# Kernel optimization log

Hardware: AMD Instinct MI355X
Metric: run time of the kernel (lower is better)

Reference implementation:

```python
import jax, jax.numpy as jnp
import numpy as np

B, CLEN, QLEN, H = 16, 4096, 512, 256


def setup_inputs() -> dict:
    key = jax.random.key(0)
    ks = jax.random.split(key, 8)
    scale = 1.0 / np.sqrt(H)
    return {
        "c": jax.random.normal(ks[0], (B, CLEN, H), dtype=jnp.float32),
        "q": jax.random.normal(ks[1], (B, QLEN, H), dtype=jnp.float32),
        "w_c": jax.random.normal(ks[2], (H,), dtype=jnp.float32) * scale,
        "b_c": jax.random.normal(ks[3], (), dtype=jnp.float32) * scale,
        "w_q": jax.random.normal(ks[4], (H,), dtype=jnp.float32) * scale,
        "b_q": jax.random.normal(ks[5], (), dtype=jnp.float32) * scale,
        "w_cq": jax.random.normal(ks[6], (H,), dtype=jnp.float32) * scale,
        "b_cq": jax.random.normal(ks[7], (), dtype=jnp.float32) * scale,
    }


def reference(c, q, w_c, b_c, w_q, b_q, w_cq, b_cq):
    # Trilinear similarity: s[b,i,j] = c_i.w_c + q_j.w_q + sum_d w_cq[d]*c[b,i,d]*q[b,j,d] + biases
    cq = jnp.einsum("bid,bjd->bij", c * w_cq, q) + b_cq          # (B, c_len, q_len)
    s = (c @ w_c + b_c)[:, :, None] + (q @ w_q + b_q)[:, None, :] + cq
    # context-to-query attention
    a = jax.nn.softmax(s, axis=2)                                  # (B, c_len, q_len)
    c2q_att = jnp.einsum("bij,bjd->bid", a, q)                     # (B, c_len, H)
    # query-to-context attention (max over queries, softmax over context)
    b_att = jax.nn.softmax(jnp.max(s, axis=2), axis=1)             # (B, c_len)
    q2c_att = jnp.einsum("bi,bid->bd", b_att, c)[:, None, :]       # (B, 1, H)
    q2c_att = jnp.broadcast_to(q2c_att, c.shape)                   # (B, c_len, H)
    x = jnp.concatenate([c, c2q_att, c * c2q_att, c * q2c_att], axis=2)
    return x  # (B, c_len, 4*H)
```

## Files before the change

kernel.cpp:

```cpp
#include <hip/hip_runtime.h>
#include <hip/hip_fp16.h>

constexpr int NB = 16;
constexpr int CL = 4096;
constexpr int QL = 512;
constexpr int HD = 256;

typedef _Float16 f16x8 __attribute__((ext_vector_type(8)));
typedef _Float16 f16x4 __attribute__((ext_vector_type(4)));
typedef float    f32x4 __attribute__((ext_vector_type(4)));


__global__ void k_prep_q(const float* __restrict__ q, const float* __restrict__ w_q,
                         const float* __restrict__ b_q, const float* __restrict__ w_cq,
                         const float* __restrict__ b_cq,
                         _Float16* __restrict__ qph, float* __restrict__ qd2) {
    int row  = blockIdx.x * 4 + (threadIdx.x >> 6);
    int lane = threadIdx.x & 63;
    float4 qv  = ((const float4*)(q + (size_t)row * HD))[lane];
    float4 wq  = ((const float4*)w_q)[lane];
    float4 wcq = ((const float4*)w_cq)[lane];
    f16x4 hv = {(_Float16)(qv.x * wcq.x), (_Float16)(qv.y * wcq.y),
                (_Float16)(qv.z * wcq.z), (_Float16)(qv.w * wcq.w)};
    *(f16x4*)(qph + (size_t)row * HD + lane * 4) = hv;
    float s = qv.x * wq.x + qv.y * wq.y + qv.z * wq.z + qv.w * wq.w;
    #pragma unroll
    for (int off = 32; off; off >>= 1) s += __shfl_down(s, off, 64);
    if (lane == 0) qd2[row] = s + b_q[0] + b_cq[0];
}

__global__ void k_cdot(const float* __restrict__ c, const float* __restrict__ w_c,
                       const float* __restrict__ b_c, float* __restrict__ cdot) {
    int row  = blockIdx.x * 4 + (threadIdx.x >> 6);
    int lane = threadIdx.x & 63;
    float4 cv = ((const float4*)(c + (size_t)row * HD))[lane];
    float4 wv = ((const float4*)w_c)[lane];
    float s = cv.x * wv.x + cv.y * wv.y + cv.z * wv.z + cv.w * wv.w;
    #pragma unroll
    for (int off = 32; off; off >>= 1) s += __shfl_down(s, off, 64);
    if (lane == 0) cdot[row] = s + b_c[0];
}

__global__ void k_tq(const float* __restrict__ q, _Float16* __restrict__ qth) {
    __shared__ float tile[64][65];
    int b  = blockIdx.z;
    int d0 = blockIdx.x * 64;
    int j0 = blockIdx.y * 64;
    int t  = threadIdx.x;
    int rr = t >> 4, cseg = t & 15;
    #pragma unroll
    for (int p = 0; p < 4; ++p) {
        int r = rr + p * 16;
        float4 v = *(const float4*)(q + ((size_t)b * QL + j0 + r) * HD + d0 + cseg * 4);
        tile[r][cseg * 4 + 0] = v.x; tile[r][cseg * 4 + 1] = v.y;
        tile[r][cseg * 4 + 2] = v.z; tile[r][cseg * 4 + 3] = v.w;
    }
    __syncthreads();
    #pragma unroll
    for (int p = 0; p < 4; ++p) {
        int dr = rr + p * 16;
        f16x4 hv = {(_Float16)tile[cseg * 4 + 0][dr], (_Float16)tile[cseg * 4 + 1][dr],
                    (_Float16)tile[cseg * 4 + 2][dr], (_Float16)tile[cseg * 4 + 3][dr]};
        *(f16x4*)(qth + ((size_t)b * HD + d0 + dr) * QL + j0 + cseg * 4) = hv;
    }
}

__launch_bounds__(512, 4)
__global__ void k_fused(const float* __restrict__ c, const _Float16* __restrict__ qph,
                        const float* __restrict__ qd2, const _Float16* __restrict__ qth,
                        float* __restrict__ rowmax, float* __restrict__ x) {
    __shared__ __align__(1024) char smem[65536];

    const int b  = blockIdx.y;
    const int i0 = blockIdx.x * 64;
    const int t  = threadIdx.x;
    const int wave = t >> 6;
    const int ln   = t & 15;
    const int quad = (t >> 4) & 3;
    const int jw   = wave;

    f32x4 acc[4][4];
    #pragma unroll
    for (int mt = 0; mt < 4; ++mt)
        #pragma unroll
        for (int nt = 0; nt < 4; ++nt) acc[mt][nt] = (f32x4){0.f, 0.f, 0.f, 0.f};

    for (int dc = 0; dc < 4; ++dc) {
        __syncthreads();
        {
            const int row = t >> 3, seg = t & 7;
            #pragma unroll
            for (int p = 0; p < 8; ++p) {
                int j = row + p * 64;
                f16x8 hv = *(const f16x8*)(qph + ((size_t)b * QL + j) * HD + dc * 64 + seg * 8);
                int byte = (j << 7) + (seg << 4);
                byte ^= (j & 7) << 4;
                *(f16x8*)(smem + byte) = hv;
            }
        }
        __syncthreads();
        #pragma unroll
        for (int ks = 0; ks < 2; ++ks) {
            f16x8 bf[4];
            #pragma unroll
            for (int nt = 0; nt < 4; ++nt) {
                const float* src = c + ((size_t)b * CL + i0 + nt * 16 + ln) * HD
                                     + dc * 64 + ks * 32 + quad * 8;
                float4 v0 = *(const float4*)src;
                float4 v1 = *(const float4*)(src + 4);
                bf[nt] = (f16x8){(_Float16)v0.x, (_Float16)v0.y, (_Float16)v0.z, (_Float16)v0.w,
                                 (_Float16)v1.x, (_Float16)v1.y, (_Float16)v1.z, (_Float16)v1.w};
            }
            #pragma unroll
            for (int mt = 0; mt < 4; ++mt) {
                int j = jw * 64 + mt * 16 + ln;
                int byte = (j << 7) + (ks * 64 + quad * 16);
                byte ^= (j & 7) << 4;
                f16x8 af = *(const f16x8*)(smem + byte);
                #pragma unroll
                for (int nt = 0; nt < 4; ++nt)
                    acc[mt][nt] = __builtin_amdgcn_mfma_f32_16x16x32_f16(af, bf[nt], acc[mt][nt], 0, 0, 0);
            }
        }
    }

    float m[4];
    #pragma unroll
    for (int nt = 0; nt < 4; ++nt) m[nt] = -1e30f;
    #pragma unroll
    for (int mt = 0; mt < 4; ++mt) {
        float4 qv = *(const float4*)(qd2 + b * QL + jw * 64 + mt * 16 + quad * 4);
        #pragma unroll
        for (int nt = 0; nt < 4; ++nt) {
            acc[mt][nt][0] += qv.x; acc[mt][nt][1] += qv.y;
            acc[mt][nt][2] += qv.z; acc[mt][nt][3] += qv.w;
            m[nt] = fmaxf(m[nt], fmaxf(fmaxf(acc[mt][nt][0], acc[mt][nt][1]),
                                       fmaxf(acc[mt][nt][2], acc[mt][nt][3])));
        }
    }
    #pragma unroll
    for (int nt = 0; nt < 4; ++nt) {
        m[nt] = fmaxf(m[nt], __shfl_xor(m[nt], 16, 64));
        m[nt] = fmaxf(m[nt], __shfl_xor(m[nt], 32, 64));
    }
    __syncthreads();
    float* redM = (float*)smem;
    float* redZ = (float*)(smem + 2048);
    if (quad == 0) {
        #pragma unroll
        for (int nt = 0; nt < 4; ++nt) redM[jw * 64 + nt * 16 + ln] = m[nt];
    }
    __syncthreads();
    #pragma unroll
    for (int nt = 0; nt < 4; ++nt) {
        int ri = nt * 16 + ln;
        float mm = redM[ri];
        #pragma unroll
        for (int w = 1; w < 8; ++w) mm = fmaxf(mm, redM[w * 64 + ri]);
        m[nt] = mm;
    }
    if (jw == 0 && quad == 0) {
        #pragma unroll
        for (int nt = 0; nt < 4; ++nt)
            rowmax[(size_t)b * CL + i0 + nt * 16 + ln] = m[nt];
    }
    float z[4] = {0.f, 0.f, 0.f, 0.f};
    #pragma unroll
    for (int mt = 0; mt < 4; ++mt)
        #pragma unroll
        for (int nt = 0; nt < 4; ++nt) {
            #pragma unroll
            for (int r = 0; r < 4; ++r) {
                float e = __expf(acc[mt][nt][r] - m[nt]);
                acc[mt][nt][r] = e;
                z[nt] += e;
            }
        }
    #pragma unroll
    for (int nt = 0; nt < 4; ++nt) {
        z[nt] += __shfl_xor(z[nt], 16, 64);
        z[nt] += __shfl_xor(z[nt], 32, 64);
    }
    if (quad == 0) {
        #pragma unroll
        for (int nt = 0; nt < 4; ++nt) redZ[jw * 64 + nt * 16 + ln] = z[nt];
    }
    __syncthreads();
    float inv[4];
    #pragma unroll
    for (int nt = 0; nt < 4; ++nt) {
        int ri = nt * 16 + ln;
        float zz = redZ[ri];
        #pragma unroll
        for (int w = 1; w < 8; ++w) zz += redZ[w * 64 + ri];
        inv[nt] = 1.0f / zz;
    }
    __syncthreads();

    #pragma unroll
    for (int mt = 0; mt < 4; ++mt) {
        int jcol = jw * 64 + mt * 16 + quad * 4;
        #pragma unroll
        for (int nt = 0; nt < 4; ++nt) {
            int i = nt * 16 + ln;
            f16x4 hv = {(_Float16)(acc[mt][nt][0] * inv[nt]),
                        (_Float16)(acc[mt][nt][1] * inv[nt]),
                        (_Float16)(acc[mt][nt][2] * inv[nt]),
                        (_Float16)(acc[mt][nt][3] * inv[nt])};
            int byte = (i << 10) + (jcol << 1);
            byte ^= (i & 7) << 4;
            *(f16x4*)(smem + byte) = hv;
        }
    }
    __syncthreads();

    const int iw = wave >> 2;
    const int dw = wave & 3;
    f32x4 acc2[2][4];
    #pragma unroll
    for (int it = 0; it < 2; ++it)
        #pragma unroll
        for (int dt = 0; dt < 4; ++dt) acc2[it][dt] = (f32x4){0.f, 0.f, 0.f, 0.f};

    const _Float16* qthb = qth + (size_t)b * HD * QL;
    #pragma unroll 4
    for (int kc = 0; kc < 16; ++kc) {
        f16x8 af[2], bf[4];
        #pragma unroll
        for (int it = 0; it < 2; ++it) {
            int i = iw * 32 + it * 16 + ln;
            int byte = (i << 10) + (kc * 64 + quad * 16);
            byte ^= (i & 7) << 4;
            af[it] = *(const f16x8*)(smem + byte);
        }
        #pragma unroll
        for (int dt = 0; dt < 4; ++dt)
            bf[dt] = *(const f16x8*)(qthb + (size_t)(dw * 64 + dt * 16 + ln) * QL
                                     + kc * 32 + quad * 8);
        #pragma unroll
        for (int it = 0; it < 2; ++it)
            #pragma unroll
            for (int dt = 0; dt < 4; ++dt)
                acc2[it][dt] = __builtin_amdgcn_mfma_f32_16x16x32_f16(af[it], bf[dt], acc2[it][dt], 0, 0, 0);
    }

    #pragma unroll
    for (int it = 0; it < 2; ++it) {
        #pragma unroll
        for (int r = 0; r < 4; ++r) {
            int i = i0 + iw * 32 + it * 16 + quad * 4 + r;
            const float* crow = c + ((size_t)b * CL + i) * HD;
            float* xrow = x + ((size_t)b * CL + i) * (4 * HD);
            #pragma unroll
            for (int dt = 0; dt < 4; ++dt) {
                int d = dw * 64 + dt * 16 + ln;
                float cv = crow[d];
                float a  = acc2[it][dt][r];
                xrow[HD + d]     = a;
                xrow[2 * HD + d] = cv * a;
            }
        }
    }
}

__global__ void k_batch_mz(const float* __restrict__ rowmax, const float* __restrict__ cdot,
                           float* __restrict__ Mb, float* __restrict__ Zb,
                           float* __restrict__ q2c) {
    int b = blockIdx.x, t = threadIdx.x;
    q2c[b * HD + t] = 0.f;
    float vals[16];
    float m = -1e30f;
    #pragma unroll
    for (int k = 0; k < 16; ++k) {
        int i = t + k * 256;
        vals[k] = rowmax[b * CL + i] + cdot[b * CL + i];
        m = fmaxf(m, vals[k]);
    }
    __shared__ float redm[4], redz[4];
    #pragma unroll
    for (int off = 32; off; off >>= 1) m = fmaxf(m, __shfl_xor(m, off, 64));
    if ((t & 63) == 0) redm[t >> 6] = m;
    __syncthreads();
    m = fmaxf(fmaxf(redm[0], redm[1]), fmaxf(redm[2], redm[3]));
    float z = 0.f;
    #pragma unroll
    for (int k = 0; k < 16; ++k) z += __expf(vals[k] - m);
    #pragma unroll
    for (int off = 32; off; off >>= 1) z += __shfl_xor(z, off, 64);
    if ((t & 63) == 0) redz[t >> 6] = z;
    __syncthreads();
    if (t == 0) { Mb[b] = m; Zb[b] = redz[0] + redz[1] + redz[2] + redz[3]; }
}

__global__ void k_q2c(const float* __restrict__ c, const float* __restrict__ rowmax,
                      const float* __restrict__ cdot, const float* __restrict__ Mb,
                      const float* __restrict__ Zb, float* __restrict__ q2c) {
    int b = blockIdx.x >> 6, slab = blockIdx.x & 63;
    int dd = threadIdx.x;
    float M = Mb[b], invZ = 1.0f / Zb[b];
    float acc = 0.f;
    for (int r = 0; r < 64; ++r) {
        int i = slab * 64 + r;
        float w = __expf(rowmax[b * CL + i] + cdot[b * CL + i] - M);
        acc += w * c[((size_t)b * CL + i) * HD + dd];
    }
    atomicAdd(&q2c[b * HD + dd], acc * invZ);
}

__global__ void k_x03(const float* __restrict__ c, const float* __restrict__ q2c,
                      float* __restrict__ x) {
    int row  = blockIdx.x * 4 + (threadIdx.x >> 6);
    int lane = threadIdx.x & 63;
    int b = row >> 12;
    float4 cv = ((const float4*)(c + (size_t)row * HD))[lane];
    float4 qv = ((const float4*)(q2c + b * HD))[lane];
    float4 o  = {cv.x * qv.x, cv.y * qv.y, cv.z * qv.z, cv.w * qv.w};
    float* xrow = x + (size_t)row * (4 * HD);
    ((float4*)xrow)[lane]            = cv;
    ((float4*)(xrow + 3 * HD))[lane] = o;
}

extern "C" void kernel_launch(void* const* d_in, const int* in_sizes, int n_in,
                              void* d_out, int out_size, void* d_ws, size_t ws_size,
                              hipStream_t stream) {
    const float* c    = (const float*)d_in[0];
    const float* q    = (const float*)d_in[1];
    const float* w_c  = (const float*)d_in[2];
    const float* b_c  = (const float*)d_in[3];
    const float* w_q  = (const float*)d_in[4];
    const float* b_q  = (const float*)d_in[5];
    const float* w_cq = (const float*)d_in[6];
    const float* b_cq = (const float*)d_in[7];
    float* x = (float*)d_out;

    char* ws = (char*)d_ws;
    _Float16* qph  = (_Float16*)(ws);
    _Float16* qth  = (_Float16*)(ws + 4194304);
    float*  qd2    = (float*)(ws + 8388608);
    float*  cdot   = (float*)(ws + 8421376);
    float*  rowmax = (float*)(ws + 8683520);
    float*  Mb     = (float*)(ws + 8945664);
    float*  Zb     = (float*)(ws + 8945728);
    float*  q2c    = (float*)(ws + 8945792);

    k_prep_q<<<NB * QL / 4, 256, 0, stream>>>(q, w_q, b_q, w_cq, b_cq, qph, qd2);
    k_cdot<<<NB * CL / 4, 256, 0, stream>>>(c, w_c, b_c, cdot);
    k_tq<<<dim3(HD / 64, QL / 64, NB), 256, 0, stream>>>(q, qth);
    k_fused<<<dim3(CL / 64, NB), 512, 0, stream>>>(c, qph, qd2, qth, rowmax, x);
    k_batch_mz<<<NB, 256, 0, stream>>>(rowmax, cdot, Mb, Zb, q2c);
    k_q2c<<<NB * 64, 256, 0, stream>>>(c, rowmax, cdot, Mb, Zb, q2c);
    k_x03<<<NB * CL / 4, 256, 0, stream>>>(c, q2c, x);
}
```

Before: 490.1 us.

## Double-buffer per-wave q tiles via direct global-to-LDS loads without block barriers

Replaces the block-wide staged copy of q·w_cq into LDS with per-wave private slices. Each slice is filled by global_load_lds direct-to-LDS transfers, double-buffered across eight 32-wide d-chunks and ordered with s_waitcnt vmcnt instead of __syncthreads. The aim is to overlap the next chunk's q fetch with the current MFMA work and to drop barrier and register round-trip costs. It also loosens launch bounds from 4 to 2 blocks per CU, giving the compiler more registers at the cost of guaranteed occupancy. Correctness depends on the vmcnt counts matching the number of outstanding loads.

```diff
diff --git a/kernel.cpp b/kernel.cpp
--- a/kernel.cpp
+++ b/kernel.cpp
@@ -9,6 +9,9 @@
 typedef _Float16 f16x8 __attribute__((ext_vector_type(8)));
 typedef _Float16 f16x4 __attribute__((ext_vector_type(4)));
 typedef float    f32x4 __attribute__((ext_vector_type(4)));
+
+typedef __attribute__((address_space(3))) void lds_void;
+typedef __attribute__((address_space(1))) const void glb_void;
 
 
 __global__ void k_prep_q(const float* __restrict__ q, const float* __restrict__ w_q,
@@ -65,7 +68,7 @@
     }
 }
 
-__launch_bounds__(512, 4)
+__launch_bounds__(512, 2)
 __global__ void k_fused(const float* __restrict__ c, const _Float16* __restrict__ qph,
                         const float* __restrict__ qd2, const _Float16* __restrict__ qth,
                         float* __restrict__ rowmax, float* __restrict__ x) {
@@ -75,52 +78,61 @@
     const int i0 = blockIdx.x * 64;
     const int t  = threadIdx.x;
     const int wave = t >> 6;
+    const int l    = t & 63;
     const int ln   = t & 15;
     const int quad = (t >> 4) & 3;
     const int jw   = wave;
 
+    const int srcseg = (l & 3) ^ ((l >> 3) & 3);
+    const _Float16* qpb = qph + ((size_t)b * QL + jw * 64) * HD;
+
     f32x4 acc[4][4];
     #pragma unroll
     for (int mt = 0; mt < 4; ++mt)
         #pragma unroll
         for (int nt = 0; nt < 4; ++nt) acc[mt][nt] = (f32x4){0.f, 0.f, 0.f, 0.f};
 
-    for (int dc = 0; dc < 4; ++dc) {
-        __syncthreads();
-        {
-            const int row = t >> 3, seg = t & 7;
-            #pragma unroll
-            for (int p = 0; p < 8; ++p) {
-                int j = row + p * 64;
-                f16x8 hv = *(const f16x8*)(qph + ((size_t)b * QL + j) * HD + dc * 64 + seg * 8);
-                int byte = (j << 7) + (seg << 4);
-                byte ^= (j & 7) << 4;
-                *(f16x8*)(smem + byte) = hv;
+    #pragma unroll
+    for (int p = 0; p < 4; ++p) {
+        const _Float16* src = qpb + (size_t)(p * 16 + (l >> 2)) * HD + srcseg * 8;
+        char* dst = smem + jw * 4096 + p * 1024;
+        __builtin_amdgcn_global_load_lds((glb_void*)src, (lds_void*)dst, 16, 0, 0);
+    }
+
+    const int xq = (ln >> 1) & 3;
+    for (int ch = 0; ch < 8; ++ch) {
+        if (ch < 7) {
+            const int buf = (ch + 1) & 1;
+            #pragma unroll
+            for (int p = 0; p < 4; ++p) {
+                const _Float16* src = qpb + (size_t)(p * 16 + (l >> 2)) * HD
+                                    + (ch + 1) * 32 + srcseg * 8;
+                char* dst = smem + buf * 32768 + jw * 4096 + p * 1024;
+                __builtin_amdgcn_global_load_lds((glb_void*)src, (lds_void*)dst, 16, 0, 0);
             }
-        }
-        __syncthreads();
-        #pragma unroll
-        for (int ks = 0; ks < 2; ++ks) {
-            f16x8 bf[4];
-            #pragma unroll
-            for (int nt = 0; nt < 4; ++nt) {
-                const float* src = c + ((size_t)b * CL + i0 + nt * 16 + ln) * HD
-                                     + dc * 64 + ks * 32 + quad * 8;
-                float4 v0 = *(const float4*)src;
-                float4 v1 = *(const float4*)(src + 4);
-                bf[nt] = (f16x8){(_Float16)v0.x, (_Float16)v0.y, (_Float16)v0.z, (_Float16)v0.w,
-                                 (_Float16)v1.x, (_Float16)v1.y, (_Float16)v1.z, (_Float16)v1.w};
-            }
-            #pragma unroll
-            for (int mt = 0; mt < 4; ++mt) {
-                int j = jw * 64 + mt * 16 + ln;
-                int byte = (j << 7) + (ks * 64 + quad * 16);
-                byte ^= (j & 7) << 4;
-                f16x8 af = *(const f16x8*)(smem + byte);
-                #pragma unroll
-                for (int nt = 0; nt < 4; ++nt)
-                    acc[mt][nt] = __builtin_amdgcn_mfma_f32_16x16x32_f16(af, bf[nt], acc[mt][nt], 0, 0, 0);
-            }
+            asm volatile("s_waitcnt vmcnt(4)" ::: "memory");
+        } else {
+            asm volatile("s_waitcnt vmcnt(0)" ::: "memory");
+        }
+        f16x8 bf[4];
+        #pragma unroll
+        for (int nt = 0; nt < 4; ++nt) {
+            const float* srcc = c + ((size_t)b * CL + i0 + nt * 16 + ln) * HD
+                              + ch * 32 + quad * 8;
+            float4 v0 = *(const float4*)srcc;
+            float4 v1 = *(const float4*)(srcc + 4);
+            bf[nt] = (f16x8){(_Float16)v0.x, (_Float16)v0.y, (_Float16)v0.z, (_Float16)v0.w,
+                             (_Float16)v1.x, (_Float16)v1.y, (_Float16)v1.z, (_Float16)v1.w};
+        }
+        #pragma unroll
+        for (int mt = 0; mt < 4; ++mt) {
+            int rr = mt * 16 + ln;
+            const char* ap = smem + (ch & 1) * 32768 + jw * 4096 + rr * 64
+                           + ((quad ^ xq) << 4);
+            f16x8 af = *(const f16x8*)ap;
+            #pragma unroll
+            for (int nt = 0; nt < 4; ++nt)
+                acc[mt][nt] = __builtin_amdgcn_mfma_f32_16x16x32_f16(af, bf[nt], acc[mt][nt], 0, 0, 0);
         }
     }
 
```

After: 472.3 us. -3.6%, faster.

## Double context tile per block to 128 rows with 2x4 wave grid

Applied to the files above, without the earlier changes.

The fused attention kernel now processes 128 context rows per block instead of 64. Its 8 waves are split into a 2x4 grid over context rows and query columns, and each wave accumulates 8x4 MFMA tiles. The q tile is staged in 32-wide chunks with padded rows instead of the XOR swizzle. Softmax probabilities stay in registers and are written to LDS in two halves for the second GEMM. This halves the number of times qph and qth are reloaded across blocks. The cost is much higher register pressure (launch bounds drop to 2 blocks per CU), lower occupancy and fewer blocks in the grid.

```diff
diff --git a/kernel.cpp b/kernel.cpp
--- a/kernel.cpp
+++ b/kernel.cpp
@@ -65,71 +65,68 @@
     }
 }
 
-__launch_bounds__(512, 4)
+__launch_bounds__(512, 2)
 __global__ void k_fused(const float* __restrict__ c, const _Float16* __restrict__ qph,
                         const float* __restrict__ qd2, const _Float16* __restrict__ qth,
                         float* __restrict__ rowmax, float* __restrict__ x) {
-    __shared__ __align__(1024) char smem[65536];
+    __shared__ __align__(64) char smem[65536];
+    _Float16 (*qphL)[40] = (_Float16 (*)[40])smem;
 
     const int b  = blockIdx.y;
-    const int i0 = blockIdx.x * 64;
+    const int i0 = blockIdx.x * 128;
     const int t  = threadIdx.x;
     const int wave = t >> 6;
+    const int wi = wave >> 2;
+    const int wj = wave & 3;
     const int ln   = t & 15;
     const int quad = (t >> 4) & 3;
-    const int jw   = wave;
-
-    f32x4 acc[4][4];
-    #pragma unroll
-    for (int mt = 0; mt < 4; ++mt)
+
+    f32x4 acc[8][4];
+    #pragma unroll
+    for (int mt = 0; mt < 8; ++mt)
         #pragma unroll
         for (int nt = 0; nt < 4; ++nt) acc[mt][nt] = (f32x4){0.f, 0.f, 0.f, 0.f};
 
-    for (int dc = 0; dc < 4; ++dc) {
+    for (int ch = 0; ch < 8; ++ch) {
         __syncthreads();
-        {
-            const int row = t >> 3, seg = t & 7;
-            #pragma unroll
-            for (int p = 0; p < 8; ++p) {
-                int j = row + p * 64;
-                f16x8 hv = *(const f16x8*)(qph + ((size_t)b * QL + j) * HD + dc * 64 + seg * 8);
-                int byte = (j << 7) + (seg << 4);
-                byte ^= (j & 7) << 4;
-                *(f16x8*)(smem + byte) = hv;
-            }
+        #pragma unroll
+        for (int p = 0; p < 4; ++p) {
+            int seg = t + p * 512;
+            int row = seg >> 2, s = seg & 3;
+            f16x8 hv = *(const f16x8*)(qph + ((size_t)b * QL + row) * HD + ch * 32 + s * 8);
+            *(f16x8*)&qphL[row][s * 8] = hv;
         }
         __syncthreads();
-        #pragma unroll
-        for (int ks = 0; ks < 2; ++ks) {
-            f16x8 bf[4];
-            #pragma unroll
-            for (int nt = 0; nt < 4; ++nt) {
-                const float* src = c + ((size_t)b * CL + i0 + nt * 16 + ln) * HD
-                                     + dc * 64 + ks * 32 + quad * 8;
-                float4 v0 = *(const float4*)src;
-                float4 v1 = *(const float4*)(src + 4);
-                bf[nt] = (f16x8){(_Float16)v0.x, (_Float16)v0.y, (_Float16)v0.z, (_Float16)v0.w,
-                                 (_Float16)v1.x, (_Float16)v1.y, (_Float16)v1.z, (_Float16)v1.w};
-            }
-            #pragma unroll
-            for (int mt = 0; mt < 4; ++mt) {
-                int j = jw * 64 + mt * 16 + ln;
-                int byte = (j << 7) + (ks * 64 + quad * 16);
-                byte ^= (j & 7) << 4;
-                f16x8 af = *(const f16x8*)(smem + byte);
-                #pragma unroll
-                for (int nt = 0; nt < 4; ++nt)
-                    acc[mt][nt] = __builtin_amdgcn_mfma_f32_16x16x32_f16(af, bf[nt], acc[mt][nt], 0, 0, 0);
-            }
-        }
-    }
+        f16x8 bf[4];
+        #pragma unroll
+        for (int nt = 0; nt < 4; ++nt) {
+            const float* srcc = c + ((size_t)b * CL + i0 + wi * 64 + nt * 16 + ln) * HD
+                              + ch * 32 + quad * 8;
+            float4 v0 = *(const float4*)srcc;
+            float4 v1 = *(const float4*)(srcc + 4);
+            bf[nt] = (f16x8){(_Float16)v0.x, (_Float16)v0.y, (_Float16)v0.z, (_Float16)v0.w,
+                             (_Float16)v1.x, (_Float16)v1.y, (_Float16)v1.z, (_Float16)v1.w};
+        }
+        #pragma unroll
+        for (int mt = 0; mt < 8; ++mt) {
+            f16x8 af = *(const f16x8*)&qphL[wj * 128 + mt * 16 + ln][quad * 8];
+            #pragma unroll
+            for (int nt = 0; nt < 4; ++nt)
+                acc[mt][nt] = __builtin_amdgcn_mfma_f32_16x16x32_f16(af, bf[nt], acc[mt][nt], 0, 0, 0);
+        }
+    }
+    __syncthreads();
+
+    float* redM = (float*)smem;
+    float* redZ = (float*)(smem + 2048);
+    const int il = wi * 64 + (t & 15);
 
     float m[4];
     #pragma unroll
     for (int nt = 0; nt < 4; ++nt) m[nt] = -1e30f;
     #pragma unroll
-    for (int mt = 0; mt < 4; ++mt) {
-        float4 qv = *(const float4*)(qd2 + b * QL + jw * 64 + mt * 16 + quad * 4);
+    for (int mt = 0; mt < 8; ++mt) {
+        float4 qv = *(const float4*)(qd2 + b * QL + wj * 128 + mt * 16 + quad * 4);
         #pragma unroll
         for (int nt = 0; nt < 4; ++nt) {
             acc[mt][nt][0] += qv.x; acc[mt][nt][1] += qv.y;
@@ -143,30 +140,26 @@
         m[nt] = fmaxf(m[nt], __shfl_xor(m[nt], 16, 64));
         m[nt] = fmaxf(m[nt], __shfl_xor(m[nt], 32, 64));
     }
-    __syncthreads();
-    float* redM = (float*)smem;
-    float* redZ = (float*)(smem + 2048);
     if (quad == 0) {
         #pragma unroll
-        for (int nt = 0; nt < 4; ++nt) redM[jw * 64 + nt * 16 + ln] = m[nt];
+        for (int nt = 0; nt < 4; ++nt) redM[wj * 128 + il + nt * 16] = m[nt];
     }
     __syncthreads();
     #pragma unroll
     for (int nt = 0; nt < 4; ++nt) {
-        int ri = nt * 16 + ln;
-        float mm = redM[ri];
-        #pragma unroll
-        for (int w = 1; w < 8; ++w) mm = fmaxf(mm, redM[w * 64 + ri]);
+        float mm = redM[il + nt * 16];
+        #pragma unroll
+        for (int w = 1; w < 4; ++w) mm = fmaxf(mm, redM[w * 128 + il + nt * 16]);
         m[nt] = mm;
     }
-    if (jw == 0 && quad == 0) {
+    if (wj == 0 && quad == 0) {
         #pragma unroll
         for (int nt = 0; nt < 4; ++nt)
-            rowmax[(size_t)b * CL + i0 + nt * 16 + ln] = m[nt];
+            rowmax[(size_t)b * CL + i0 + il + nt * 16] = m[nt];
     }
     float z[4] = {0.f, 0.f, 0.f, 0.f};
     #pragma unroll
-    for (int mt = 0; mt < 4; ++mt)
+    for (int mt = 0; mt < 8; ++mt)
         #pragma unroll
         for (int nt = 0; nt < 4; ++nt) {
             #pragma unroll
@@ -183,77 +176,85 @@
     }
     if (quad == 0) {
         #pragma unroll
-        for (int nt = 0; nt < 4; ++nt) redZ[jw * 64 + nt * 16 + ln] = z[nt];
-    }
-    __syncthreads();
-    float inv[4];
-    #pragma unroll
-    for (int nt = 0; nt < 4; ++nt) {
-        int ri = nt * 16 + ln;
-        float zz = redZ[ri];
-        #pragma unroll
-        for (int w = 1; w < 8; ++w) zz += redZ[w * 64 + ri];
-        inv[nt] = 1.0f / zz;
-    }
-    __syncthreads();
-
-    #pragma unroll
-    for (int mt = 0; mt < 4; ++mt) {
-        int jcol = jw * 64 + mt * 16 + quad * 4;
+        for (int nt = 0; nt < 4; ++nt) redZ[wj * 128 + il + nt * 16] = z[nt];
+    }
+    __syncthreads();
+    f16x4 ph[8][4];
+    {
+        float inv[4];
         #pragma unroll
         for (int nt = 0; nt < 4; ++nt) {
-            int i = nt * 16 + ln;
-            f16x4 hv = {(_Float16)(acc[mt][nt][0] * inv[nt]),
-                        (_Float16)(acc[mt][nt][1] * inv[nt]),
-                        (_Float16)(acc[mt][nt][2] * inv[nt]),
-                        (_Float16)(acc[mt][nt][3] * inv[nt])};
-            int byte = (i << 10) + (jcol << 1);
-            byte ^= (i & 7) << 4;
-            *(f16x4*)(smem + byte) = hv;
-        }
-    }
-    __syncthreads();
-
-    const int iw = wave >> 2;
-    const int dw = wave & 3;
-    f32x4 acc2[2][4];
-    #pragma unroll
-    for (int it = 0; it < 2; ++it)
+            float zz = redZ[il + nt * 16];
+            #pragma unroll
+            for (int w = 1; w < 4; ++w) zz += redZ[w * 128 + il + nt * 16];
+            inv[nt] = 1.0f / zz;
+        }
+        #pragma unroll
+        for (int mt = 0; mt < 8; ++mt)
+            #pragma unroll
+            for (int nt = 0; nt < 4; ++nt)
+                ph[mt][nt] = (f16x4){(_Float16)(acc[mt][nt][0] * inv[nt]),
+                                     (_Float16)(acc[mt][nt][1] * inv[nt]),
+                                     (_Float16)(acc[mt][nt][2] * inv[nt]),
+                                     (_Float16)(acc[mt][nt][3] * inv[nt])};
+    }
+
+    f32x4 acc2[4][4];
+    #pragma unroll
+    for (int it = 0; it < 4; ++it)
         #pragma unroll
         for (int dt = 0; dt < 4; ++dt) acc2[it][dt] = (f32x4){0.f, 0.f, 0.f, 0.f};
 
     const _Float16* qthb = qth + (size_t)b * HD * QL;
-    #pragma unroll 4
-    for (int kc = 0; kc < 16; ++kc) {
-        f16x8 af[2], bf[4];
-        #pragma unroll
-        for (int it = 0; it < 2; ++it) {
-            int i = iw * 32 + it * 16 + ln;
-            int byte = (i << 10) + (kc * 64 + quad * 16);
-            byte ^= (i & 7) << 4;
-            af[it] = *(const f16x8*)(smem + byte);
-        }
-        #pragma unroll
-        for (int dt = 0; dt < 4; ++dt)
-            bf[dt] = *(const f16x8*)(qthb + (size_t)(dw * 64 + dt * 16 + ln) * QL
-                                     + kc * 32 + quad * 8);
-        #pragma unroll
-        for (int it = 0; it < 2; ++it)
+    #pragma unroll
+    for (int p = 0; p < 2; ++p) {
+        __syncthreads();
+        if ((wj >> 1) == p) {
+            #pragma unroll
+            for (int mt = 0; mt < 8; ++mt) {
+                int jl = (wj & 1) * 128 + mt * 16 + quad * 4;
+                #pragma unroll
+                for (int nt = 0; nt < 4; ++nt) {
+                    int i = il + nt * 16;
+                    int byte = (i << 9) + (jl << 1);
+                    byte ^= (i & 7) << 4;
+                    *(f16x4*)(smem + byte) = ph[mt][nt];
+                }
+            }
+        }
+        __syncthreads();
+        #pragma unroll 2
+        for (int kc = 0; kc < 8; ++kc) {
+            f16x8 af[4], bf[4];
+            #pragma unroll
+            for (int it = 0; it < 4; ++it) {
+                int i = wi * 64 + it * 16 + ln;
+                int byte = (i << 9) + kc * 64 + quad * 16;
+                byte ^= (i & 7) << 4;
+                af[it] = *(const f16x8*)(smem + byte);
+            }
             #pragma unroll
             for (int dt = 0; dt < 4; ++dt)
-                acc2[it][dt] = __builtin_amdgcn_mfma_f32_16x16x32_f16(af[it], bf[dt], acc2[it][dt], 0, 0, 0);
-    }
-
-    #pragma unroll
-    for (int it = 0; it < 2; ++it) {
+                bf[dt] = *(const f16x8*)(qthb + (size_t)(wj * 64 + dt * 16 + ln) * QL
+                                         + p * 256 + kc * 32 + quad * 8);
+            #pragma unroll
+            for (int it = 0; it < 4; ++it)
+                #pragma unroll
+                for (int dt = 0; dt < 4; ++dt)
+                    acc2[it][dt] = __builtin_amdgcn_mfma_f32_16x16x32_f16(af[it], bf[dt], acc2[it][dt], 0, 0, 0);
+        }
+    }
+
+    #pragma unroll
+    for (int it = 0; it < 4; ++it) {
         #pragma unroll
         for (int r = 0; r < 4; ++r) {
-            int i = i0 + iw * 32 + it * 16 + quad * 4 + r;
+            int i = i0 + wi * 64 + it * 16 + quad * 4 + r;
             const float* crow = c + ((size_t)b * CL + i) * HD;
             float* xrow = x + ((size_t)b * CL + i) * (4 * HD);
             #pragma unroll
             for (int dt = 0; dt < 4; ++dt) {
-                int d = dw * 64 + dt * 16 + ln;
+                int d = wj * 64 + dt * 16 + ln;
                 float cv = crow[d];
                 float a  = acc2[it][dt][r];
                 xrow[HD + d]     = a;
@@ -346,7 +347,7 @@
     k_prep_q<<<NB * QL / 4, 256, 0, stream>>>(q, w_q, b_q, w_cq, b_cq, qph, qd2);
     k_cdot<<<NB * CL / 4, 256, 0, stream>>>(c, w_c, b_c, cdot);
     k_tq<<<dim3(HD / 64, QL / 64, NB), 256, 0, stream>>>(q, qth);
-    k_fused<<<dim3(CL / 64, NB), 512, 0, stream>>>(c, qph, qd2, qth, rowmax, x);
+    k_fused<<<dim3(CL / 128, NB), 512, 0, stream>>>(c, qph, qd2, qth, rowmax, x);
     k_batch_mz<<<NB, 256, 0, stream>>>(rowmax, cdot, Mb, Zb, q2c);
     k_q2c<<<NB * 64, 256, 0, stream>>>(c, rowmax, cdot, Mb, Zb, q2c);
     k_x03<<<NB * CL / 4, 256, 0, stream>>>(c, q2c, x);
```

Measured after the change: 450.9 us. 1.09x faster.
